# Performance work log

Measured on AMD Instinct MI355X. Metric: run time of the kernel, lower is better.

Reference implementation:

```python
import jax, jax.numpy as jnp
import numpy as np

EMBED_DIM = 768
NUM_HEADS = 12
HEAD_DIM = EMBED_DIM // NUM_HEADS
D_FF = 4 * EMBED_DIM
EPS = 1e-6


def setup_inputs() -> dict:
    key = jax.random.key(0)
    ks = jax.random.split(key, 16)
    B, N, D = 4, 1024, EMBED_DIM
    s = 0.02
    return {
        "x": jax.random.normal(ks[0], (B, N, D), jnp.float32),
        "ln1_g": jnp.ones((D,), jnp.float32),
        "ln1_b": jnp.zeros((D,), jnp.float32),
        "Wq": jax.random.normal(ks[1], (D, D), jnp.float32) * s,
        "bq": jnp.zeros((D,), jnp.float32),
        "Wk": jax.random.normal(ks[2], (D, D), jnp.float32) * s,
        "bk": jnp.zeros((D,), jnp.float32),
        "Wv": jax.random.normal(ks[3], (D, D), jnp.float32) * s,
        "bv": jnp.zeros((D,), jnp.float32),
        "Wo": jax.random.normal(ks[4], (D, D), jnp.float32) * s,
        "bo": jnp.zeros((D,), jnp.float32),
        "ln2_g": jnp.ones((D,), jnp.float32),
        "ln2_b": jnp.zeros((D,), jnp.float32),
        "W1": jax.random.normal(ks[5], (D, D_FF), jnp.float32) * s,
        "b1": jnp.zeros((D_FF,), jnp.float32),
        "W2": jax.random.normal(ks[6], (D_FF, D), jnp.float32) * s,
        "b2": jnp.zeros((D,), jnp.float32),
    }


def _layernorm(x, g, b):
    mu = jnp.mean(x, axis=-1, keepdims=True)
    var = jnp.mean(jnp.square(x - mu), axis=-1, keepdims=True)
    return (x - mu) * jax.lax.rsqrt(var + EPS) * g + b


def _block(x, ln1_g, ln1_b, Wq, bq, Wk, bk, Wv, bv, Wo, bo,
           ln2_g, ln2_b, W1, b1, W2, b2):
    B, N, D = x.shape
    h = x
    xn = _layernorm(x, ln1_g, ln1_b)
    # [B, H, N, d]
    q = (xn @ Wq + bq).reshape(B, N, NUM_HEADS, HEAD_DIM).transpose(0, 2, 1, 3)
    k = (xn @ Wk + bk).reshape(B, N, NUM_HEADS, HEAD_DIM).transpose(0, 2, 1, 3)
    v = (xn @ Wv + bv).reshape(B, N, NUM_HEADS, HEAD_DIM).transpose(0, 2, 1, 3)
    scores = jnp.einsum('bhqd,bhkd->bhqk', q, k) / np.sqrt(HEAD_DIM).astype(x.dtype)
    probs = jax.nn.softmax(scores, axis=-1)
    ctx = jnp.einsum('bhqk,bhkd->bhqd', probs, v)
    ctx = ctx.transpose(0, 2, 1, 3).reshape(B, N, D)
    attn_out = ctx @ Wo + bo
    x = attn_out + h
    h = x
    xn = _layernorm(x, ln2_g, ln2_b)
    mlp = jax.nn.gelu(xn @ W1 + b1, approximate=False) @ W2 + b2
    return mlp + h


def reference(x, ln1_g, ln1_b, Wq, bq, Wk, bk, Wv, bv, Wo, bo,
              ln2_g, ln2_b, W1, b1, W2, b2):
    return _block(x, ln1_g, ln1_b, Wq, bq, Wk, bk, Wv, bv, Wo, bo,
                  ln2_g, ln2_b, W1, b1, W2, b2)
```

## Files before the change

### kernel.cpp

```cpp
#include <hip/hip_runtime.h>

typedef __bf16 bf16_t;
typedef bf16_t bf16x8 __attribute__((ext_vector_type(8)));
typedef float f32x4 __attribute__((ext_vector_type(4)));
typedef unsigned short us8 __attribute__((ext_vector_type(8)));

#define DEV static __device__ __forceinline__

DEV unsigned short f2bf(float f) {
  unsigned int x = __float_as_uint(f);
  return (unsigned short)((x + 0x7fffu + ((x >> 16) & 1u)) >> 16);
}

DEV f32x4 mfma16(bf16x8 a, bf16x8 b, f32x4 c) {
  return __builtin_amdgcn_mfma_f32_16x16x32_bf16(a, b, c, 0, 0, 0);
}

DEV void gload_lds16(const void* g, void* l) {
  __builtin_amdgcn_global_load_lds(
      (const __attribute__((address_space(1))) void*)g,
      (__attribute__((address_space(3))) void*)l, 16, 0, 0);
}

__global__ __launch_bounds__(256) void wt_transpose(
    const float* __restrict__ src, unsigned short* __restrict__ dst, int K, int N) {
  __shared__ float tile[32][33];
  int bx = blockIdx.x * 32;
  int by = blockIdx.y * 32;
  int tx = threadIdx.x, ty = threadIdx.y;
#pragma unroll
  for (int i = ty; i < 32; i += 8)
    tile[i][tx] = src[(size_t)(by + i) * N + bx + tx];
  __syncthreads();
#pragma unroll
  for (int i = ty; i < 32; i += 8)
    dst[(size_t)(bx + i) * K + by + tx] = f2bf(tile[tx][i]);
}

__global__ __launch_bounds__(256) void ln_kernel(
    const float* __restrict__ x, const float* __restrict__ gw,
    const float* __restrict__ bw, unsigned short* __restrict__ out) {
  int row = blockIdx.x;
  const float* xr = x + (size_t)row * 768;
  int t = threadIdx.x;
  float v0 = xr[t], v1 = xr[t + 256], v2 = xr[t + 512];
  float s = v0 + v1 + v2, sq = v0 * v0 + v1 * v1 + v2 * v2;
#pragma unroll
  for (int m = 1; m < 64; m <<= 1) { s += __shfl_xor(s, m); sq += __shfl_xor(sq, m); }
  __shared__ float ssum[4], ssq[4];
  int wid = t >> 6;
  if ((t & 63) == 0) { ssum[wid] = s; ssq[wid] = sq; }
  __syncthreads();
  s = ssum[0] + ssum[1] + ssum[2] + ssum[3];
  sq = ssq[0] + ssq[1] + ssq[2] + ssq[3];
  float mu = s * (1.f / 768.f);
  float var = sq * (1.f / 768.f) - mu * mu;
  float rstd = rsqrtf(fmaxf(var, 0.f) + 1e-6f);
  unsigned short* orow = out + (size_t)row * 768;
  orow[t]       = f2bf((v0 - mu) * rstd * gw[t]       + bw[t]);
  orow[t + 256] = f2bf((v1 - mu) * rstd * gw[t + 256] + bw[t + 256]);
  orow[t + 512] = f2bf((v2 - mu) * rstd * gw[t + 512] + bw[t + 512]);
}

template <int EPI>
__global__ __launch_bounds__(256) void gemm_bt(
    const unsigned short* __restrict__ A, const unsigned short* __restrict__ Bt, int K,
    const float* __restrict__ b0p, const float* __restrict__ b1p, const float* __restrict__ b2p,
    const float* __restrict__ resid,
    void* __restrict__ o0, void* __restrict__ o1, void* __restrict__ o2) {
  __shared__ unsigned short lA[128 * 32];
  __shared__ unsigned short lB[128 * 32];
  int tid = threadIdx.x;
  int wid = tid >> 6, lane = tid & 63;
  int bm = blockIdx.y * 128, bn = blockIdx.x * 128;
  int wr = (wid >> 1) * 64, wc = (wid & 1) * 64;

  f32x4 acc[4][4] = {};

  const unsigned short* ga  = A  + (size_t)(bm + (tid >> 2)) * K + (tid & 3) * 8;
  const unsigned short* ga2 = A  + (size_t)(bm + 64 + (tid >> 2)) * K + (tid & 3) * 8;
  const unsigned short* gb  = Bt + (size_t)(bn + (tid >> 2)) * K + (tid & 3) * 8;
  const unsigned short* gb2 = Bt + (size_t)(bn + 64 + (tid >> 2)) * K + (tid & 3) * 8;

  for (int kt = 0; kt < K; kt += 32) {
    __syncthreads();
    gload_lds16(ga,  (char*)lA + wid * 1024);
    gload_lds16(ga2, (char*)lA + 4096 + wid * 1024);
    gload_lds16(gb,  (char*)lB + wid * 1024);
    gload_lds16(gb2, (char*)lB + 4096 + wid * 1024);
    ga += 32; ga2 += 32; gb += 32; gb2 += 32;
    __syncthreads();
    bf16x8 af[4], bfv[4];
#pragma unroll
    for (int mi = 0; mi < 4; mi++)
      af[mi] = *(const bf16x8*)(lA + (wr + mi * 16 + (lane & 15)) * 32 + (lane >> 4) * 8);
#pragma unroll
    for (int ni = 0; ni < 4; ni++)
      bfv[ni] = *(const bf16x8*)(lB + (wc + ni * 16 + (lane & 15)) * 32 + (lane >> 4) * 8);
#pragma unroll
    for (int mi = 0; mi < 4; mi++)
#pragma unroll
      for (int ni = 0; ni < 4; ni++)
        acc[mi][ni] = mfma16(af[mi], bfv[ni], acc[mi][ni]);
  }

  int r0 = bm + wr + ((lane >> 4) << 2);
  int c0 = bn + wc + (lane & 15);
#pragma unroll
  for (int mi = 0; mi < 4; mi++) {
#pragma unroll
    for (int ni = 0; ni < 4; ni++) {
      int col = c0 + ni * 16;
#pragma unroll
      for (int r = 0; r < 4; r++) {
        int row = r0 + mi * 16 + r;
        float val = acc[mi][ni][r];
        if constexpr (EPI == 0) {
          int which = col / 768;
          int rem = col - which * 768;
          int h = rem >> 6, d = rem & 63;
          const float* bias = (which == 0) ? b0p : (which == 1) ? b1p : b2p;
          unsigned short* dst = (unsigned short*)((which == 0) ? o0 : (which == 1) ? o1 : o2);
          val += bias[rem];
          if (which == 0) val *= 0.125f;
          int b = row >> 10, n = row & 1023;
          dst[(((size_t)b * 12 + h) * 1024 + n) * 64 + d] = f2bf(val);
        } else if constexpr (EPI == 1) {
          ((float*)o0)[(size_t)row * 768 + col] = val + b0p[col] + resid[(size_t)row * 768 + col];
        } else if constexpr (EPI == 2) {
          float hv = val + b0p[col];
          float ge = 0.5f * hv * (1.f + erff(hv * 0.70710678118654752f));
          ((unsigned short*)o0)[(size_t)row * 3072 + col] = f2bf(ge);
        } else {
          ((float*)o0)[(size_t)row * 768 + col] = val + b0p[col] + resid[(size_t)row * 768 + col];
        }
      }
    }
  }
}

__global__ __launch_bounds__(256) void attn_kernel(
    const unsigned short* __restrict__ q, const unsigned short* __restrict__ k,
    const unsigned short* __restrict__ v, unsigned short* __restrict__ ctx) {
  int bh = blockIdx.y;
  int bb = bh / 12, hh = bh % 12;
  int q0 = blockIdx.x * 64;
  int wid = threadIdx.x >> 6, lane = threadIdx.x & 63;
  const size_t head_off = (size_t)bh * 1024 * 64;
  const unsigned short* qh = q + head_off;
  const unsigned short* kh = k + head_off;
  const unsigned short* vh = v + head_off;

  __shared__ unsigned short lK[64 * 64];
  __shared__ unsigned short lVt[64][72];
  __shared__ unsigned short lP[4][16][72];

  bf16x8 aq[2];
  {
    int row = q0 + wid * 16 + (lane & 15);
    const unsigned short* qr = qh + (size_t)row * 64 + (lane >> 4) * 8;
    aq[0] = *(const bf16x8*)qr;
    aq[1] = *(const bf16x8*)(qr + 32);
  }
  f32x4 cacc[4] = {};
  float mrow[4], lrow[4];
#pragma unroll
  for (int r = 0; r < 4; r++) { mrow[r] = -1e30f; lrow[r] = 0.f; }

  for (int kt = 0; kt < 16; ++kt) {
    __syncthreads();
    {
      int t = threadIdx.x;
      int row = t >> 3;
      int colb = (t & 7) * 16;
      const unsigned short* g0 = kh + (size_t)(kt * 64 + row) * 64 + ((colb ^ ((row & 7) << 4)) >> 1);
      gload_lds16(g0, (char*)lK + wid * 1024);
      int row2 = row + 32;
      const unsigned short* g1 = kh + (size_t)(kt * 64 + row2) * 64 + ((colb ^ ((row & 7) << 4)) >> 1);
      gload_lds16(g1, (char*)lK + 4096 + wid * 1024);
    }
    {
      int kp = threadIdx.x >> 3;
      int d0 = (threadIdx.x & 7) * 8;
      const unsigned short* vp = vh + (size_t)(kt * 64 + kp * 2) * 64 + d0;
      us8 r0v = *(const us8*)vp;
      us8 r1v = *(const us8*)(vp + 64);
      unsigned int* lv = (unsigned int*)lVt;
#pragma unroll
      for (int j = 0; j < 8; j++)
        lv[(d0 + j) * 36 + kp] = (unsigned int)r0v[j] | ((unsigned int)r1v[j] << 16);
    }
    __syncthreads();

    f32x4 sacc[4] = {};
#pragma unroll
    for (int ni = 0; ni < 4; ni++) {
      int krow = ni * 16 + (lane & 15);
      int swz = (krow & 7) << 4;
      const char* base = (const char*)lK + krow * 128;
      bf16x8 b0 = *(const bf16x8*)(base + (((lane >> 4) * 16) ^ swz));
      bf16x8 b1 = *(const bf16x8*)(base + ((64 + (lane >> 4) * 16) ^ swz));
      sacc[ni] = mfma16(aq[0], b0, sacc[ni]);
      sacc[ni] = mfma16(aq[1], b1, sacc[ni]);
    }

    float pv[4][4];
#pragma unroll
    for (int r = 0; r < 4; r++) {
      float tm = fmaxf(fmaxf(sacc[0][r], sacc[1][r]), fmaxf(sacc[2][r], sacc[3][r]));
#pragma unroll
      for (int m = 1; m < 16; m <<= 1) tm = fmaxf(tm, __shfl_xor(tm, m));
      float mn = fmaxf(mrow[r], tm);
      float corr = __expf(mrow[r] - mn);
      float rs = 0.f;
#pragma unroll
      for (int ni = 0; ni < 4; ni++) {
        float p = __expf(sacc[ni][r] - mn);
        pv[ni][r] = p;
        rs += p;
      }
#pragma unroll
      for (int m = 1; m < 16; m <<= 1) rs += __shfl_xor(rs, m);
      lrow[r] = lrow[r] * corr + rs;
      mrow[r] = mn;
#pragma unroll
      for (int di = 0; di < 4; di++) cacc[di][r] *= corr;
    }

#pragma unroll
    for (int ni = 0; ni < 4; ni++)
#pragma unroll
      for (int r = 0; r < 4; r++)
        lP[wid][(lane >> 4) * 4 + r][ni * 16 + (lane & 15)] = f2bf(pv[ni][r]);

#pragma unroll
    for (int kc = 0; kc < 2; kc++) {
      bf16x8 pa = *(const bf16x8*)&lP[wid][lane & 15][kc * 32 + (lane >> 4) * 8];
#pragma unroll
      for (int di = 0; di < 4; di++) {
        bf16x8 bvv = *(const bf16x8*)&lVt[di * 16 + (lane & 15)][kc * 32 + (lane >> 4) * 8];
        cacc[di] = mfma16(pa, bvv, cacc[di]);
      }
    }
  }

#pragma unroll
  for (int di = 0; di < 4; di++)
#pragma unroll
    for (int r = 0; r < 4; r++)
      lP[wid][(lane >> 4) * 4 + r][di * 16 + (lane & 15)] = f2bf(cacc[di][r] / lrow[r]);
  {
    int row = lane >> 2;
    int c0 = (lane & 3) * 16;
    const unsigned short* sp = &lP[wid][row][c0];
    us8 w0 = *(const us8*)sp;
    us8 w1 = *(const us8*)(sp + 8);
    int gq = q0 + wid * 16 + row;
    unsigned short* gp = ctx + ((size_t)(bb * 1024 + gq)) * 768 + hh * 64 + c0;
    *(us8*)gp = w0;
    *(us8*)(gp + 8) = w1;
  }
}

extern "C" void kernel_launch(void* const* d_in, const int* in_sizes, int n_in,
                              void* d_out, int out_size, void* d_ws, size_t ws_size,
                              hipStream_t stream) {
  const float* x    = (const float*)d_in[0];
  const float* ln1g = (const float*)d_in[1];
  const float* ln1b = (const float*)d_in[2];
  const float* Wq   = (const float*)d_in[3];
  const float* bq   = (const float*)d_in[4];
  const float* Wk   = (const float*)d_in[5];
  const float* bk   = (const float*)d_in[6];
  const float* Wv   = (const float*)d_in[7];
  const float* bv   = (const float*)d_in[8];
  const float* Wo   = (const float*)d_in[9];
  const float* bo   = (const float*)d_in[10];
  const float* ln2g = (const float*)d_in[11];
  const float* ln2b = (const float*)d_in[12];
  const float* W1   = (const float*)d_in[13];
  const float* b1   = (const float*)d_in[14];
  const float* W2   = (const float*)d_in[15];
  const float* b2   = (const float*)d_in[16];
  float* out = (float*)d_out;

  char* ws = (char*)d_ws;
  unsigned short* xn    = (unsigned short*)(ws + 0);
  float*          x2    = (float*)(ws + 6291456);
  unsigned short* x2n   = (unsigned short*)(ws + 18874368);
  unsigned short* qws   = (unsigned short*)(ws + 25165824);
  unsigned short* kws   = (unsigned short*)(ws + 31457280);
  unsigned short* vws   = (unsigned short*)(ws + 37748736);
  unsigned short* ctx   = (unsigned short*)(ws + 44040192);
  unsigned short* hmid  = (unsigned short*)(ws + 50331648);
  unsigned short* Wqkvt = (unsigned short*)(ws + 75497472);
  unsigned short* Wot   = (unsigned short*)(ws + 79036416);
  unsigned short* W1t   = (unsigned short*)(ws + 80216064);
  unsigned short* W2t   = (unsigned short*)(ws + 84934656);

  dim3 tb(32, 8);
  wt_transpose<<<dim3(24, 24), tb, 0, stream>>>(Wq, Wqkvt, 768, 768);
  wt_transpose<<<dim3(24, 24), tb, 0, stream>>>(Wk, Wqkvt + 589824, 768, 768);
  wt_transpose<<<dim3(24, 24), tb, 0, stream>>>(Wv, Wqkvt + 1179648, 768, 768);
  wt_transpose<<<dim3(24, 24), tb, 0, stream>>>(Wo, Wot, 768, 768);
  wt_transpose<<<dim3(96, 24), tb, 0, stream>>>(W1, W1t, 768, 3072);
  wt_transpose<<<dim3(24, 96), tb, 0, stream>>>(W2, W2t, 3072, 768);

  ln_kernel<<<4096, 256, 0, stream>>>(x, ln1g, ln1b, xn);
  gemm_bt<0><<<dim3(18, 32), 256, 0, stream>>>(xn, Wqkvt, 768, bq, bk, bv, nullptr, qws, kws, vws);
  attn_kernel<<<dim3(16, 48), 256, 0, stream>>>(qws, kws, vws, ctx);
  gemm_bt<1><<<dim3(6, 32), 256, 0, stream>>>(ctx, Wot, 768, bo, nullptr, nullptr, x, x2, nullptr, nullptr);
  ln_kernel<<<4096, 256, 0, stream>>>(x2, ln2g, ln2b, x2n);
  gemm_bt<2><<<dim3(24, 32), 256, 0, stream>>>(x2n, W1t, 768, b1, nullptr, nullptr, nullptr, hmid, nullptr, nullptr);
  gemm_bt<3><<<dim3(6, 32), 256, 0, stream>>>(hmid, W2t, 3072, b2, nullptr, nullptr, x2, out, nullptr, nullptr);
}
```

Baseline: 358.2 us.

## Split-K narrow-tile GEMM with reduction kernel for Wo and W2 projections

Replaces the 128x128-tile GEMMs for the attention output and second MLP projections (only 192 blocks on a many-CU GPU) with a 128x64-tile split-K kernel launched on a 12x32x2 grid. Partial sums go to a fp32 workspace, and a separate elementwise kernel adds the bias and residual. The goal is to fill the GPU better on these narrow N=768 GEMMs. In exchange it writes and reads extra fp32 partial buffers, adds a launch per GEMM, and reorganises the workspace layout so the partials reuse the xn/q region.

Measured after the change: 336.8 us. 1.06x faster.

```diff
diff --git a/kernel.cpp b/kernel.cpp
--- a/kernel.cpp
+++ b/kernel.cpp
@@ -66,7 +66,6 @@
 __global__ __launch_bounds__(256) void gemm_bt(
     const unsigned short* __restrict__ A, const unsigned short* __restrict__ Bt, int K,
     const float* __restrict__ b0p, const float* __restrict__ b1p, const float* __restrict__ b2p,
-    const float* __restrict__ resid,
     void* __restrict__ o0, void* __restrict__ o1, void* __restrict__ o2) {
   __shared__ unsigned short lA[128 * 32];
   __shared__ unsigned short lB[128 * 32];
@@ -125,18 +124,76 @@
           if (which == 0) val *= 0.125f;
           int b = row >> 10, n = row & 1023;
           dst[(((size_t)b * 12 + h) * 1024 + n) * 64 + d] = f2bf(val);
-        } else if constexpr (EPI == 1) {
-          ((float*)o0)[(size_t)row * 768 + col] = val + b0p[col] + resid[(size_t)row * 768 + col];
-        } else if constexpr (EPI == 2) {
+        } else {
           float hv = val + b0p[col];
           float ge = 0.5f * hv * (1.f + erff(hv * 0.70710678118654752f));
           ((unsigned short*)o0)[(size_t)row * 3072 + col] = f2bf(ge);
-        } else {
-          ((float*)o0)[(size_t)row * 768 + col] = val + b0p[col] + resid[(size_t)row * 768 + col];
         }
       }
     }
   }
+}
+
+__global__ __launch_bounds__(256) void gemm_sk(
+    const unsigned short* __restrict__ A, const unsigned short* __restrict__ Bt,
+    int K, int ksplit, float* __restrict__ part) {
+  __shared__ unsigned short lA[128 * 32];
+  __shared__ unsigned short lB[64 * 32];
+  int tid = threadIdx.x;
+  int wid = tid >> 6, lane = tid & 63;
+  int bm = blockIdx.y * 128, bn = blockIdx.x * 64;
+  int k0 = blockIdx.z * ksplit;
+  int wr = (wid >> 1) * 64, wc = (wid & 1) * 32;
+
+  f32x4 acc[4][2] = {};
+
+  const unsigned short* ga  = A  + (size_t)(bm + (tid >> 2)) * K + k0 + (tid & 3) * 8;
+  const unsigned short* ga2 = A  + (size_t)(bm + 64 + (tid >> 2)) * K + k0 + (tid & 3) * 8;
+  const unsigned short* gb  = Bt + (size_t)(bn + (tid >> 2)) * K + k0 + (tid & 3) * 8;
+
+  for (int kt = 0; kt < ksplit; kt += 32) {
+    __syncthreads();
+    gload_lds16(ga,  (char*)lA + wid * 1024);
+    gload_lds16(ga2, (char*)lA + 4096 + wid * 1024);
+    gload_lds16(gb,  (char*)lB + wid * 1024);
+    ga += 32; ga2 += 32; gb += 32;
+    __syncthreads();
+    bf16x8 af[4], bfv[2];
+#pragma unroll
+    for (int mi = 0; mi < 4; mi++)
+      af[mi] = *(const bf16x8*)(lA + (wr + mi * 16 + (lane & 15)) * 32 + (lane >> 4) * 8);
+#pragma unroll
+    for (int ni = 0; ni < 2; ni++)
+      bfv[ni] = *(const bf16x8*)(lB + (wc + ni * 16 + (lane & 15)) * 32 + (lane >> 4) * 8);
+#pragma unroll
+    for (int mi = 0; mi < 4; mi++)
+#pragma unroll
+      for (int ni = 0; ni < 2; ni++)
+        acc[mi][ni] = mfma16(af[mi], bfv[ni], acc[mi][ni]);
+  }
+
+  float* pp = part + (size_t)blockIdx.z * (4096 * 768);
+  int r0 = bm + wr + ((lane >> 4) << 2);
+  int c0 = bn + wc + (lane & 15);
+#pragma unroll
+  for (int mi = 0; mi < 4; mi++)
+#pragma unroll
+    for (int ni = 0; ni < 2; ni++)
+#pragma unroll
+      for (int r = 0; r < 4; r++)
+        pp[(size_t)(r0 + mi * 16 + r) * 768 + c0 + ni * 16] = acc[mi][ni][r];
+}
+
+__global__ __launch_bounds__(256) void skred(
+    const float* __restrict__ part, const float* __restrict__ bias,
+    const float* __restrict__ resid, float* __restrict__ out) {
+  int i = blockIdx.x * 256 + threadIdx.x;
+  const f32x4* p0 = (const f32x4*)part;
+  const f32x4* p1 = p0 + 786432;
+  const f32x4* rz = (const f32x4*)resid;
+  const f32x4* bz = (const f32x4*)bias;
+  f32x4 v = p0[i] + p1[i] + bz[i % 192] + rz[i];
+  ((f32x4*)out)[i] = v;
 }
 
 __global__ __launch_bounds__(256) void attn_kernel(
@@ -286,12 +343,13 @@
 
   char* ws = (char*)d_ws;
   unsigned short* xn    = (unsigned short*)(ws + 0);
-  float*          x2    = (float*)(ws + 6291456);
-  unsigned short* x2n   = (unsigned short*)(ws + 18874368);
-  unsigned short* qws   = (unsigned short*)(ws + 25165824);
-  unsigned short* kws   = (unsigned short*)(ws + 31457280);
-  unsigned short* vws   = (unsigned short*)(ws + 37748736);
-  unsigned short* ctx   = (unsigned short*)(ws + 44040192);
+  unsigned short* qws   = (unsigned short*)(ws + 6291456);
+  unsigned short* kws   = (unsigned short*)(ws + 12582912);
+  unsigned short* vws   = (unsigned short*)(ws + 18874368);
+  float*          part  = (float*)(ws + 0);
+  unsigned short* ctx   = (unsigned short*)(ws + 25165824);
+  float*          x2    = (float*)(ws + 31457280);
+  unsigned short* x2n   = (unsigned short*)(ws + 44040192);
   unsigned short* hmid  = (unsigned short*)(ws + 50331648);
   unsigned short* Wqkvt = (unsigned short*)(ws + 75497472);
   unsigned short* Wot   = (unsigned short*)(ws + 79036416);
@@ -307,10 +365,12 @@
   wt_transpose<<<dim3(24, 96), tb, 0, stream>>>(W2, W2t, 3072, 768);
 
   ln_kernel<<<4096, 256, 0, stream>>>(x, ln1g, ln1b, xn);
-  gemm_bt<0><<<dim3(18, 32), 256, 0, stream>>>(xn, Wqkvt, 768, bq, bk, bv, nullptr, qws, kws, vws);
+  gemm_bt<0><<<dim3(18, 32), 256, 0, stream>>>(xn, Wqkvt, 768, bq, bk, bv, qws, kws, vws);
   attn_kernel<<<dim3(16, 48), 256, 0, stream>>>(qws, kws, vws, ctx);
-  gemm_bt<1><<<dim3(6, 32), 256, 0, stream>>>(ctx, Wot, 768, bo, nullptr, nullptr, x, x2, nullptr, nullptr);
+  gemm_sk<<<dim3(12, 32, 2), 256, 0, stream>>>(ctx, Wot, 768, 384, part);
+  skred<<<3072, 256, 0, stream>>>(part, bo, x, x2);
   ln_kernel<<<4096, 256, 0, stream>>>(x2, ln2g, ln2b, x2n);
-  gemm_bt<2><<<dim3(24, 32), 256, 0, stream>>>(x2n, W1t, 768, b1, nullptr, nullptr, nullptr, hmid, nullptr, nullptr);
-  gemm_bt<3><<<dim3(6, 32), 256, 0, stream>>>(hmid, W2t, 3072, b2, nullptr, nullptr, x2, out, nullptr, nullptr);
-}
+  gemm_bt<2><<<dim3(24, 32), 256, 0, stream>>>(x2n, W1t, 768, b1, nullptr, nullptr, hmid, nullptr, nullptr);
+  gemm_sk<<<dim3(12, 32, 2), 256, 0, stream>>>(hmid, W2t, 3072, 1536, part);
+  skred<<<3072, 256, 0, stream>>>(part, b2, x2, out);
+}
```
